# Kernel tuning notes

Measured on AMD Instinct MI355X. Metric: run time of the kernel, lower is better.

## Reference

```python
import jax, jax.numpy as jnp
import numpy as np

B, S, H, N = 4, 512, 768, 128
MAX_SPAN_WIDTH = 10
WIDTH_DIM = 30


def setup_inputs() -> dict:
    key = jax.random.key(0)
    ks = jax.random.split(key, 20)
    p = lambda k, shape: jax.random.normal(k, shape, jnp.float32) * 0.02
    starts = jax.random.randint(ks[1], (B, N), 0, S, dtype=jnp.int32)
    widths = jax.random.randint(ks[2], (B, N), 0, MAX_SPAN_WIDTH + 1, dtype=jnp.int32)
    ends = jnp.clip(starts + widths, 0, S - 1)
    return {
        "sequence_output": jax.random.normal(ks[0], (B, S, H), jnp.float32),
        "span_starts": starts,
        "span_ends": ends,
        # SpanRepresentation params (weights stored as [in, out], i.e. torch W.T)
        "W_start": p(ks[3], (H, H)), "b_start": p(ks[4], (H,)),
        "W_end": p(ks[5], (H, H)), "b_end": p(ks[6], (H,)),
        "width_emb": p(ks[7], (MAX_SPAN_WIDTH + 1, WIDTH_DIM)),
        "W_out": p(ks[8], (2 * H + WIDTH_DIM, H)), "b_out": p(ks[9], (H,)),
        # MentionScorer head
        "W_ment": p(ks[10], (H, 1)), "b_ment": p(ks[11], (1,)),
        # PairwiseScorer 2-layer MLP over concat([r_i, r_j, r_i - r_j])
        "W1": p(ks[12], (3 * H, H)), "b1": p(ks[13], (H,)),
        "W2": p(ks[14], (H, 1)), "b2": p(ks[15], (1,)),
    }


def reference(sequence_output, span_starts, span_ends,
              W_start, b_start, W_end, b_end, width_emb, W_out, b_out,
              W_ment, b_ment, W1, b1, W2, b2):
    bidx = jnp.arange(sequence_output.shape[0])[:, None]            # [B,1]
    # --- SpanRepresentation ---
    start_embed = sequence_output[bidx, span_starts] @ W_start + b_start  # [B,N,H]
    end_embed = sequence_output[bidx, span_ends] @ W_end + b_end          # [B,N,H]
    widths = jnp.clip(span_ends - span_starts, 0, MAX_SPAN_WIDTH)
    w_embed = width_emb[widths]                                           # [B,N,WD]
    span_repr = jnp.concatenate([start_embed, end_embed, w_embed], -1) @ W_out + b_out  # [B,N,H]
    # --- MentionScorer ---
    mention_scores = (span_repr @ W_ment + b_ment)[..., 0]               # [B,N]
    # --- PairwiseScorer: ffn(cat([r_i, r_j, r_i - r_j])) for j < i ---
    # cat([ri, rj, ri-rj]) @ W1 == ri@(Wa+Wc) + rj@(Wb-Wc), with W1 = [Wa;Wb;Wc]
    Wa, Wb, Wc = W1[:H], W1[H:2 * H], W1[2 * H:]
    Ai = span_repr @ (Wa + Wc)                                           # [B,N,H]
    Bj = span_repr @ (Wb - Wc)                                           # [B,N,H]
    hidden = jax.nn.relu(Ai[:, :, None, :] + Bj[:, None, :, :] + b1)     # [B,N,N,H]
    pw = (hidden @ W2)[..., 0] + b2[0]                                   # [B,N,N]
    lower = jnp.tril(jnp.ones((pw.shape[-1], pw.shape[-1]), bool), -1)
    pairwise_scores = jnp.where(lower, pw, jnp.zeros((), pw.dtype))
    return mention_scores, pairwise_scores
```

## Files before the change

kernel.cpp:

```cpp
#include <hip/hip_runtime.h>
#include <hip/hip_bf16.h>

#define H 768
#define K2P 1600
#define SEQLEN 512
#define NSPAN 128

typedef __attribute__((ext_vector_type(8))) short s16x8;
typedef __attribute__((ext_vector_type(4))) float f32x4;

#define MFMA_BF16 __builtin_amdgcn_mfma_f32_16x16x32_bf16

__device__ __forceinline__ short f2bf(float f) {
    __hip_bfloat16 h = __float2bfloat16(f);
    return *reinterpret_cast<short*>(&h);
}
__device__ __forceinline__ float bf2f(short s) {
    unsigned int u = ((unsigned int)(unsigned short)s) << 16;
    return __builtin_bit_cast(float, u);
}

#define SLOAD(P, K0)                                                           \
    P##0 = *(const s16x8*)(gA0 + (K0));                                        \
    P##1 = *(const s16x8*)(gA1 + (K0));                                        \
    P##2 = *(const s16x8*)(gB0 + (K0));                                        \
    P##3 = *(const s16x8*)(gB1 + (K0));

#define SWRITE(P, BUF)                                                         \
    *(s16x8*)((BUF) + dA0) = P##0;                                             \
    *(s16x8*)((BUF) + dA1) = P##1;                                             \
    *(s16x8*)((BUF) + dB0) = P##2;                                             \
    *(s16x8*)((BUF) + dB1) = P##3;

__device__ __forceinline__ void mstep32(const char* buf, int w, int r, int hi,
                                        f32x4& a0, f32x4& a1)
{
    #pragma unroll
    for (int kc = 0; kc < 2; ++kc) {
        const int ko = kc*64 + hi*16;
        const int ra0 = r, ra1 = 16 + r, rb = w*16 + r;
        s16x8 av0 = *(const s16x8*)(buf + ra0*128 + (ko ^ ((ra0 & 7) << 4)));
        s16x8 av1 = *(const s16x8*)(buf + ra1*128 + (ko ^ ((ra1 & 7) << 4)));
        s16x8 bv  = *(const s16x8*)(buf + 4096 + rb*128 + (ko ^ ((rb & 7) << 4)));
        a0 = MFMA_BF16(av0, bv, a0, 0, 0, 0);
        a1 = MFMA_BF16(av1, bv, a1, 0, 0, 0);
    }
}

__device__ __forceinline__ void gemm3232(
    short* ldsb,
    const short* __restrict__ A, int ldA, int am0,
    const short* __restrict__ Wt, int ldW, int n0,
    int nsteps, int tid,
    f32x4& a0, f32x4& a1)
{
    const int w = tid >> 6, l = tid & 63;
    const int r = l & 15, hi = l >> 4;

    const int rr = tid >> 3, sl = tid & 7;
    const short* gA0 = A + (size_t)(am0 + rr) * ldA + ((sl ^ (rr & 7)) << 3);
    const short* gA1 = A + (size_t)(am0 + rr + 16) * ldA + ((sl ^ (rr & 7)) << 3);
    const short* gB0 = Wt + (size_t)(n0 + rr) * ldW + ((sl ^ (rr & 7)) << 3);
    const short* gB1 = Wt + (size_t)(n0 + rr + 16) * ldW + ((sl ^ (rr & 7)) << 3);
    const int dA0 = rr*128 + sl*16,        dA1 = (rr+16)*128 + sl*16;
    const int dB0 = 4096 + rr*128 + sl*16, dB1 = 4096 + (rr+16)*128 + sl*16;
    char* b0 = (char*)ldsb;
    char* b1 = (char*)ldsb + 8192;

    s16x8 Pa0, Pa1, Pa2, Pa3;
    s16x8 Pb0, Pb1, Pb2, Pb3;

    SLOAD(Pa, 0)
    SWRITE(Pa, b0)
    SLOAD(Pa, 64)
    __syncthreads();
    for (int s = 0; s < nsteps; s += 2) {
        if (s + 2 < nsteps) { SLOAD(Pb, 64*(s+2)) }
        mstep32(b0, w, r, hi, a0, a1);
        if (s + 1 < nsteps) { SWRITE(Pa, b1) }
        __syncthreads();
        if (s + 1 < nsteps) {
            if (s + 3 < nsteps) { SLOAD(Pa, 64*(s+3)) }
            mstep32(b1, w, r, hi, a0, a1);
            if (s + 2 < nsteps) { SWRITE(Pb, b0) }
            __syncthreads();
        }
    }
}

__global__ __launch_bounds__(256) void k_prep(
    const float* __restrict__ seq,
    const int* __restrict__ starts, const int* __restrict__ ends,
    const float* __restrict__ Ws, const float* __restrict__ We,
    const float* __restrict__ W1, const float* __restrict__ Wout,
    const float* __restrict__ wemb,
    short* __restrict__ WtSE, short* __restrict__ WtAB,
    short* __restrict__ WtOut, short* __restrict__ Xg, short* __restrict__ Xcat)
{
    const int b = blockIdx.x;
    const int tid = threadIdx.x;

    if (b < 2304) {
        const int sec = b / 576;
        const int t = b % 576;
        const int kt = t / 24, nt = t % 24;
        __shared__ float tile[32][33];
        const int kk = tid >> 3;
        const int c4 = (tid & 7) << 2;
        const int srow = kt * 32 + kk, scol = nt * 32 + c4;
        float4 v;
        if (sec == 0)      v = *(const float4*)(Ws + (size_t)srow * H + scol);
        else if (sec == 1) v = *(const float4*)(We + (size_t)srow * H + scol);
        else {
            const float* base = W1 + (size_t)(sec == 2 ? 0 : H) * H;
            float4 u = *(const float4*)(base + (size_t)srow * H + scol);
            float4 c = *(const float4*)(W1 + (size_t)2*H*H + (size_t)srow * H + scol);
            const float sg = (sec == 2) ? 1.f : -1.f;
            v = make_float4(fmaf(sg,c.x,u.x), fmaf(sg,c.y,u.y),
                            fmaf(sg,c.z,u.z), fmaf(sg,c.w,u.w));
        }
        tile[kk][c4+0]=v.x; tile[kk][c4+1]=v.y; tile[kk][c4+2]=v.z; tile[kk][c4+3]=v.w;
        __syncthreads();
        short* dst = (sec < 2 ? WtSE : WtAB) + (size_t)(sec & 1) * H * H;
        const int nn = tid >> 3;
        short4 o;
        o.x = f2bf(tile[c4+0][nn]); o.y = f2bf(tile[c4+1][nn]);
        o.z = f2bf(tile[c4+2][nn]); o.w = f2bf(tile[c4+3][nn]);
        *(short4*)(dst + (size_t)(nt*32 + nn) * H + kt*32 + c4) = o;
    } else if (b < 3504) {
        const int t = b - 2304;
        const int nt = t / 50, kt = t % 50;
        __shared__ float tile[32][33];
        const int kk = tid >> 3;
        const int c4 = (tid & 7) << 2;
        const int srow = kt * 32 + kk, scol = nt * 32 + c4;
        float4 v = make_float4(0.f, 0.f, 0.f, 0.f);
        if (srow < 1566) v = *(const float4*)(Wout + (size_t)srow * H + scol);
        tile[kk][c4+0]=v.x; tile[kk][c4+1]=v.y; tile[kk][c4+2]=v.z; tile[kk][c4+3]=v.w;
        __syncthreads();
        const int nn = tid >> 3;
        short4 o;
        o.x = f2bf(tile[c4+0][nn]); o.y = f2bf(tile[c4+1][nn]);
        o.z = f2bf(tile[c4+2][nn]); o.w = f2bf(tile[c4+3][nn]);
        *(short4*)(WtOut + (size_t)(nt*32 + nn) * K2P + kt*32 + c4) = o;
    } else if (b < 3760) {
        const int gr = (b - 3504) * 4 + (tid >> 6);
        const int c = tid & 63;
        const int spanrow = gr & 511;
        const int idx = (gr < 512) ? starts[spanrow] : ends[spanrow];
        const size_t base = ((size_t)(spanrow >> 7) * SEQLEN + idx) * H;
        #pragma unroll
        for (int i = 0; i < 12; ++i) {
            const int col = c + i*64;
            Xg[(size_t)gr * H + col] = f2bf(seq[base + col]);
        }
    } else {
        const int t = (b - 3760) * 256 + tid;
        const int row = t >> 6, c = t & 63;
        int wd = ends[row] - starts[row];
        wd = wd < 0 ? 0 : (wd > 10 ? 10 : wd);
        Xcat[(size_t)row * K2P + 1536 + c] = (c < 30) ? f2bf(wemb[wd*30 + c]) : (short)0;
    }
}

__global__ __launch_bounds__(128) void k_g1(
    const short* __restrict__ Xg, const short* __restrict__ WtSE,
    const float* __restrict__ bs, const float* __restrict__ be,
    short* __restrict__ Xcat)
{
    __shared__ __align__(16) short lds[2][4096];
    const int tid = threadIdx.x;
    const int bm = blockIdx.x, n0 = blockIdx.y * 32;
    const int am0 = (n0 >= 768 ? 512 : 0) + bm * 32;

    f32x4 a0 = {}, a1 = {};
    gemm3232(&lds[0][0], Xg, H, am0, WtSE, H, n0, 12, tid, a0, a1);

    const int w = tid >> 6, l = tid & 63;
    const int r = l & 15, hi = l >> 4;
    const int gc = n0 + w*16 + r;
    const float bv = (gc < 768) ? bs[gc] : be[gc - 768];
    const int r0 = bm*32 + hi*4, r1 = r0 + 16;
    #pragma unroll
    for (int rg = 0; rg < 4; ++rg) {
        Xcat[(size_t)(r0 + rg) * K2P + gc] = f2bf(a0[rg] + bv);
        Xcat[(size_t)(r1 + rg) * K2P + gc] = f2bf(a1[rg] + bv);
    }
}

__global__ __launch_bounds__(128) void k_g2(
    const short* __restrict__ Xcat, const short* __restrict__ WtOut,
    const float* __restrict__ bout, short* __restrict__ SR)
{
    __shared__ __align__(16) short lds[2][4096];
    const int tid = threadIdx.x;
    const int bm = blockIdx.x, n0 = blockIdx.y * 32;

    f32x4 a0 = {}, a1 = {};
    gemm3232(&lds[0][0], Xcat, K2P, bm*32, WtOut, K2P, n0, 25, tid, a0, a1);

    const int w = tid >> 6, l = tid & 63;
    const int r = l & 15, hi = l >> 4;
    const int gc = n0 + w*16 + r;
    const float bv = bout[gc];
    const int r0 = bm*32 + hi*4, r1 = r0 + 16;
    #pragma unroll
    for (int rg = 0; rg < 4; ++rg) {
        SR[(size_t)(r0 + rg) * H + gc] = f2bf(a0[rg] + bv);
        SR[(size_t)(r1 + rg) * H + gc] = f2bf(a1[rg] + bv);
    }
}

__global__ __launch_bounds__(128) void k_g3(
    const short* __restrict__ SR, const short* __restrict__ WtAB,
    const float* __restrict__ b1, const float* __restrict__ Wm,
    const float* __restrict__ bment,
    float* __restrict__ AB, float* __restrict__ mention)
{
    const int tid = threadIdx.x;
    const int bm = blockIdx.x;

    if (blockIdx.y == 48) {
        const int w = tid >> 6, l = tid & 63;
        const int rows0 = bm*32 + w*16;
        const float bm_add = bment[0];
        for (int rr = 0; rr < 16; ++rr) {
            const int row = rows0 + rr;
            float p = 0.f;
            #pragma unroll
            for (int kk = 0; kk < 12; ++kk) {
                const int k = kk*64 + l;
                p = fmaf(bf2f(SR[(size_t)row * H + k]), Wm[k], p);
            }
            #pragma unroll
            for (int off = 32; off; off >>= 1) p += __shfl_down(p, off);
            if (l == 0) mention[row] = p + bm_add;
        }
        return;
    }

    __shared__ __align__(16) short lds[2][4096];
    const int n0 = blockIdx.y * 32;

    f32x4 a0 = {}, a1 = {};
    gemm3232(&lds[0][0], SR, H, bm*32, WtAB, H, n0, 12, tid, a0, a1);

    const int w = tid >> 6, l = tid & 63;
    const int r = l & 15, hi = l >> 4;
    const int gc = n0 + w*16 + r;
    const float bv = (gc < 768) ? b1[gc] : 0.f;
    const int r0 = bm*32 + hi*4, r1 = r0 + 16;
    #pragma unroll
    for (int rg = 0; rg < 4; ++rg) {
        AB[(size_t)(r0 + rg) * 1536 + gc] = a0[rg] + bv;
        AB[(size_t)(r1 + rg) * 1536 + gc] = a1[rg] + bv;
    }
}

__global__ __launch_bounds__(256) void k_pair(
    const float* __restrict__ AB, const float* __restrict__ W2,
    const float* __restrict__ b2, float* __restrict__ pair)
{
    const int tid = threadIdx.x;
    const int bx = blockIdx.x & 7, by = blockIdx.x >> 3;
    const int bz = blockIdx.y;

    const int tx = tid & 15, ty = tid >> 4;
    const int i = by * 16 + ty, j = bx * 16 + tx;
    float* outp = pair + ((size_t)bz * NSPAN + i) * NSPAN + j;

    if (bx > by) { *outp = 0.f; return; }

    __shared__ __align__(16) float Ais[16][68];
    __shared__ __align__(16) float Bjs[16][68];
    __shared__ __align__(16) float w2s[768];
    for (int q = tid; q < 768; q += 256) w2s[q] = W2[q];

    const int sr = tid >> 4, sc = (tid & 15) << 2;
    const float* aSrc = AB + ((size_t)bz*NSPAN + by*16 + sr)*1536 + sc;
    const float* bSrc = AB + ((size_t)bz*NSPAN + bx*16 + sr)*1536 + 768 + sc;
    float acc = 0.f;

    float4 ra = *(const float4*)(aSrc);
    float4 rb = *(const float4*)(bSrc);

    for (int ch = 0; ch < 12; ++ch) {
        __syncthreads();
        *(float4*)&Ais[sr][sc] = ra;
        *(float4*)&Bjs[sr][sc] = rb;
        __syncthreads();
        if (ch < 11) {
            ra = *(const float4*)(aSrc + (ch+1)*64);
            rb = *(const float4*)(bSrc + (ch+1)*64);
        }
        #pragma unroll
        for (int hq = 0; hq < 16; ++hq) {
            float4 a = *(const float4*)&Ais[ty][hq << 2];
            float4 b = *(const float4*)&Bjs[tx][hq << 2];
            float4 wv = *(const float4*)&w2s[ch*64 + (hq << 2)];
            acc = fmaf(fmaxf(a.x + b.x, 0.f), wv.x, acc);
            acc = fmaf(fmaxf(a.y + b.y, 0.f), wv.y, acc);
            acc = fmaf(fmaxf(a.z + b.z, 0.f), wv.z, acc);
            acc = fmaf(fmaxf(a.w + b.w, 0.f), wv.w, acc);
        }
    }
    *outp = (j < i) ? (acc + b2[0]) : 0.f;
}

extern "C" void kernel_launch(void* const* d_in, const int* in_sizes, int n_in,
                              void* d_out, int out_size, void* d_ws, size_t ws_size,
                              hipStream_t stream)
{
    const float* seq    = (const float*)d_in[0];
    const int*   starts = (const int*)  d_in[1];
    const int*   ends   = (const int*)  d_in[2];
    const float* Ws     = (const float*)d_in[3];
    const float* bs     = (const float*)d_in[4];
    const float* We     = (const float*)d_in[5];
    const float* be     = (const float*)d_in[6];
    const float* wemb   = (const float*)d_in[7];
    const float* Wout   = (const float*)d_in[8];
    const float* bout   = (const float*)d_in[9];
    const float* Wm     = (const float*)d_in[10];
    const float* bment  = (const float*)d_in[11];
    const float* W1     = (const float*)d_in[12];
    const float* b1     = (const float*)d_in[13];
    const float* W2     = (const float*)d_in[14];
    const float* b2     = (const float*)d_in[15];

    float* ws = (float*)d_ws;
    float* AB    = ws;
    short* Xg    = (short*)(ws + 786432);
    short* Xcat  = (short*)(ws + 1179648);
    short* SR    = (short*)(ws + 1589248);
    short* WtSE  = (short*)(ws + 1785856);
    short* WtAB  = (short*)(ws + 2375680);
    short* WtOut = (short*)(ws + 2965504);

    float* out_mention = (float*)d_out;
    float* out_pair    = (float*)d_out + 512;

    hipLaunchKernelGGL(k_prep, dim3(3888), dim3(256), 0, stream,
                       seq, starts, ends, Ws, We, W1, Wout, wemb,
                       WtSE, WtAB, WtOut, Xg, Xcat);
    hipLaunchKernelGGL(k_g1, dim3(16, 48), dim3(128), 0, stream,
                       Xg, WtSE, bs, be, Xcat);
    hipLaunchKernelGGL(k_g2, dim3(16, 24), dim3(128), 0, stream,
                       Xcat, WtOut, bout, SR);
    hipLaunchKernelGGL(k_g3, dim3(16, 49), dim3(128), 0, stream,
                       SR, WtAB, b1, Wm, bment, AB, out_mention);
    hipLaunchKernelGGL(k_pair, dim3(64, 4), dim3(256), 0, stream,
                       AB, W2, b2, out_pair);
}
```

Measured before the change: 46.90 us.

## Fuse span gather and start/end GEMM into prep kernel, dropping one launch

The start/end projection GEMM now reads fp32 sequence rows directly through the span indices and reads the fp32 Ws/We weights column-wise, converting to bf16 on the fly. This removes the separate gather into Xg, the transposed bf16 copies of Ws/We, and the k_g1 launch. The remaining prep work (W1 combination, Wout transpose, width embedding) runs in the same launch, which now uses 128-thread blocks. The cost is strided 8-element column loads of the weights inside the GEMM pipeline and uncoalesced fp32 traffic, in exchange for one fewer kernel boundary and less intermediate memory.

```diff
diff --git a/kernel.cpp b/kernel.cpp
--- a/kernel.cpp
+++ b/kernel.cpp
@@ -19,18 +19,18 @@
     unsigned int u = ((unsigned int)(unsigned short)s) << 16;
     return __builtin_bit_cast(float, u);
 }
-
-#define SLOAD(P, K0)                                                           \
-    P##0 = *(const s16x8*)(gA0 + (K0));                                        \
-    P##1 = *(const s16x8*)(gA1 + (K0));                                        \
-    P##2 = *(const s16x8*)(gB0 + (K0));                                        \
-    P##3 = *(const s16x8*)(gB1 + (K0));
-
-#define SWRITE(P, BUF)                                                         \
-    *(s16x8*)((BUF) + dA0) = P##0;                                             \
-    *(s16x8*)((BUF) + dA1) = P##1;                                             \
-    *(s16x8*)((BUF) + dB0) = P##2;                                             \
-    *(s16x8*)((BUF) + dB1) = P##3;
+__device__ __forceinline__ s16x8 cvt8(float4 v0, float4 v1) {
+    s16x8 r;
+    r[0] = f2bf(v0.x); r[1] = f2bf(v0.y); r[2] = f2bf(v0.z); r[3] = f2bf(v0.w);
+    r[4] = f2bf(v1.x); r[5] = f2bf(v1.y); r[6] = f2bf(v1.z); r[7] = f2bf(v1.w);
+    return r;
+}
+__device__ __forceinline__ s16x8 ldcol(const float* __restrict__ p) {
+    s16x8 t;
+    t[0] = f2bf(p[0*H]); t[1] = f2bf(p[1*H]); t[2] = f2bf(p[2*H]); t[3] = f2bf(p[3*H]);
+    t[4] = f2bf(p[4*H]); t[5] = f2bf(p[5*H]); t[6] = f2bf(p[6*H]); t[7] = f2bf(p[7*H]);
+    return t;
+}
 
 __device__ __forceinline__ void mstep32(const char* buf, int w, int r, int hi,
                                         f32x4& a0, f32x4& a1)
@@ -47,6 +47,18 @@
     }
 }
 
+#define SWRITE(P, BUF)                                                         \
+    *(s16x8*)((BUF) + dA0) = P##0;                                             \
+    *(s16x8*)((BUF) + dA1) = P##1;                                             \
+    *(s16x8*)((BUF) + dB0) = P##2;                                             \
+    *(s16x8*)((BUF) + dB1) = P##3;
+
+#define SLOAD(P, K0)                                                           \
+    P##0 = *(const s16x8*)(gA0 + (K0));                                        \
+    P##1 = *(const s16x8*)(gA1 + (K0));                                        \
+    P##2 = *(const s16x8*)(gB0 + (K0));                                        \
+    P##3 = *(const s16x8*)(gB1 + (K0));
+
 __device__ __forceinline__ void gemm3232(
     short* ldsb,
     const short* __restrict__ A, int ldA, int am0,
@@ -88,107 +100,154 @@
     }
 }
 
-__global__ __launch_bounds__(256) void k_prep(
+#define G1LOAD(P, K0)                                                          \
+    P##0 = cvt8(*(const float4*)(sA0 + (K0)), *(const float4*)(sA0 + (K0) + 4)); \
+    P##1 = cvt8(*(const float4*)(sA1 + (K0)), *(const float4*)(sA1 + (K0) + 4)); \
+    P##2 = ldcol(sB0 + (size_t)(K0) * H);                                      \
+    P##3 = ldcol(sB1 + (size_t)(K0) * H);
+
+__device__ __forceinline__ void g1pipe(
+    short* ldsb, const float* __restrict__ seq, const int* __restrict__ idx,
+    int bm, const float* __restrict__ W, int n0w, int tid,
+    f32x4& a0, f32x4& a1)
+{
+    const int w = tid >> 6, l = tid & 63;
+    const int r = l & 15, hi = l >> 4;
+
+    const int rr = tid >> 3, sl = tid & 7;
+    const int gm0 = bm*32 + rr, gm1 = gm0 + 16;
+    const float* sA0 = seq + ((size_t)((gm0 >> 7) * SEQLEN + idx[gm0])) * H
+                           + ((sl ^ (rr & 7)) << 3);
+    const float* sA1 = seq + ((size_t)((gm1 >> 7) * SEQLEN + idx[gm1])) * H
+                           + ((sl ^ (rr & 7)) << 3);
+    const int nl = tid & 31, ks0 = tid >> 5;
+    const float* sB0 = W + (size_t)(ks0 * 8) * H + n0w + nl;
+    const float* sB1 = W + (size_t)((ks0 + 4) * 8) * H + n0w + nl;
+    const int dA0 = rr*128 + sl*16, dA1 = (rr+16)*128 + sl*16;
+    const int dB0 = 4096 + nl*128 + ((ks0*16)     ^ ((nl & 7) << 4));
+    const int dB1 = 4096 + nl*128 + (((ks0+4)*16) ^ ((nl & 7) << 4));
+    char* b0 = (char*)ldsb;
+    char* b1 = (char*)ldsb + 8192;
+
+    s16x8 Pa0, Pa1, Pa2, Pa3;
+    s16x8 Pb0, Pb1, Pb2, Pb3;
+
+    G1LOAD(Pa, 0)
+    SWRITE(Pa, b0)
+    G1LOAD(Pa, 64)
+    __syncthreads();
+    for (int s = 0; s < 12; s += 2) {
+        if (s + 2 < 12) { G1LOAD(Pb, 64*(s+2)) }
+        mstep32(b0, w, r, hi, a0, a1);
+        SWRITE(Pa, b1)
+        __syncthreads();
+        {
+            if (s + 3 < 12) { G1LOAD(Pa, 64*(s+3)) }
+            mstep32(b1, w, r, hi, a0, a1);
+            if (s + 2 < 12) { SWRITE(Pb, b0) }
+            __syncthreads();
+        }
+    }
+}
+
+__global__ __launch_bounds__(128) void k1(
     const float* __restrict__ seq,
     const int* __restrict__ starts, const int* __restrict__ ends,
     const float* __restrict__ Ws, const float* __restrict__ We,
+    const float* __restrict__ bs, const float* __restrict__ be,
     const float* __restrict__ W1, const float* __restrict__ Wout,
     const float* __restrict__ wemb,
-    short* __restrict__ WtSE, short* __restrict__ WtAB,
-    short* __restrict__ WtOut, short* __restrict__ Xg, short* __restrict__ Xcat)
-{
-    const int b = blockIdx.x;
+    short* __restrict__ Xcat, short* __restrict__ WtAB,
+    short* __restrict__ WtOut)
+{
+    __shared__ __align__(16) short lds[2][4096];
+    const int bid = blockIdx.x;
     const int tid = threadIdx.x;
 
-    if (b < 2304) {
-        const int sec = b / 576;
-        const int t = b % 576;
+    if (bid < 768) {
+        const int bm = bid & 15, bn = bid >> 4;
+        const int n0 = bn * 32;
+        const int* idx = (n0 < 768) ? starts : ends;
+        const float* W = (n0 < 768) ? Ws : We;
+        const int n0w  = (n0 < 768) ? n0 : n0 - 768;
+
+        f32x4 a0 = {}, a1 = {};
+        g1pipe(&lds[0][0], seq, idx, bm, W, n0w, tid, a0, a1);
+
+        const int w = tid >> 6, l = tid & 63;
+        const int r = l & 15, hi = l >> 4;
+        const int gc = n0 + w*16 + r;
+        const float bv = (gc < 768) ? bs[gc] : be[gc - 768];
+        const int r0 = bm*32 + hi*4, r1 = r0 + 16;
+        #pragma unroll
+        for (int rg = 0; rg < 4; ++rg) {
+            Xcat[(size_t)(r0 + rg) * K2P + gc] = f2bf(a0[rg] + bv);
+            Xcat[(size_t)(r1 + rg) * K2P + gc] = f2bf(a1[rg] + bv);
+        }
+    } else if (bid < 1920) {
+        float (*tile)[33] = (float(*)[33])&lds[0][0];
+        const int sec = (bid - 768) / 576;
+        const int t = (bid - 768) % 576;
         const int kt = t / 24, nt = t % 24;
-        __shared__ float tile[32][33];
-        const int kk = tid >> 3;
         const int c4 = (tid & 7) << 2;
-        const int srow = kt * 32 + kk, scol = nt * 32 + c4;
-        float4 v;
-        if (sec == 0)      v = *(const float4*)(Ws + (size_t)srow * H + scol);
-        else if (sec == 1) v = *(const float4*)(We + (size_t)srow * H + scol);
-        else {
-            const float* base = W1 + (size_t)(sec == 2 ? 0 : H) * H;
+        const float* base = W1 + (size_t)(sec ? H : 0) * H;
+        const float sg = sec ? -1.f : 1.f;
+        #pragma unroll
+        for (int p = 0; p < 2; ++p) {
+            const int kk = p*16 + (tid >> 3);
+            const int srow = kt*32 + kk, scol = nt*32 + c4;
             float4 u = *(const float4*)(base + (size_t)srow * H + scol);
             float4 c = *(const float4*)(W1 + (size_t)2*H*H + (size_t)srow * H + scol);
-            const float sg = (sec == 2) ? 1.f : -1.f;
-            v = make_float4(fmaf(sg,c.x,u.x), fmaf(sg,c.y,u.y),
-                            fmaf(sg,c.z,u.z), fmaf(sg,c.w,u.w));
-        }
-        tile[kk][c4+0]=v.x; tile[kk][c4+1]=v.y; tile[kk][c4+2]=v.z; tile[kk][c4+3]=v.w;
-        __syncthreads();
-        short* dst = (sec < 2 ? WtSE : WtAB) + (size_t)(sec & 1) * H * H;
-        const int nn = tid >> 3;
-        short4 o;
-        o.x = f2bf(tile[c4+0][nn]); o.y = f2bf(tile[c4+1][nn]);
-        o.z = f2bf(tile[c4+2][nn]); o.w = f2bf(tile[c4+3][nn]);
-        *(short4*)(dst + (size_t)(nt*32 + nn) * H + kt*32 + c4) = o;
-    } else if (b < 3504) {
-        const int t = b - 2304;
+            tile[kk][c4+0] = fmaf(sg, c.x, u.x);
+            tile[kk][c4+1] = fmaf(sg, c.y, u.y);
+            tile[kk][c4+2] = fmaf(sg, c.z, u.z);
+            tile[kk][c4+3] = fmaf(sg, c.w, u.w);
+        }
+        __syncthreads();
+        short* dst = WtAB + (size_t)sec * H * H;
+        #pragma unroll
+        for (int p = 0; p < 2; ++p) {
+            const int nn = p*16 + (tid >> 3);
+            short4 o;
+            o.x = f2bf(tile[c4+0][nn]); o.y = f2bf(tile[c4+1][nn]);
+            o.z = f2bf(tile[c4+2][nn]); o.w = f2bf(tile[c4+3][nn]);
+            *(short4*)(dst + (size_t)(nt*32 + nn) * H + kt*32 + c4) = o;
+        }
+    } else if (bid < 3120) {
+        float (*tile)[33] = (float(*)[33])&lds[0][0];
+        const int t = bid - 1920;
         const int nt = t / 50, kt = t % 50;
-        __shared__ float tile[32][33];
-        const int kk = tid >> 3;
         const int c4 = (tid & 7) << 2;
-        const int srow = kt * 32 + kk, scol = nt * 32 + c4;
-        float4 v = make_float4(0.f, 0.f, 0.f, 0.f);
-        if (srow < 1566) v = *(const float4*)(Wout + (size_t)srow * H + scol);
-        tile[kk][c4+0]=v.x; tile[kk][c4+1]=v.y; tile[kk][c4+2]=v.z; tile[kk][c4+3]=v.w;
-        __syncthreads();
-        const int nn = tid >> 3;
-        short4 o;
-        o.x = f2bf(tile[c4+0][nn]); o.y = f2bf(tile[c4+1][nn]);
-        o.z = f2bf(tile[c4+2][nn]); o.w = f2bf(tile[c4+3][nn]);
-        *(short4*)(WtOut + (size_t)(nt*32 + nn) * K2P + kt*32 + c4) = o;
-    } else if (b < 3760) {
-        const int gr = (b - 3504) * 4 + (tid >> 6);
-        const int c = tid & 63;
-        const int spanrow = gr & 511;
-        const int idx = (gr < 512) ? starts[spanrow] : ends[spanrow];
-        const size_t base = ((size_t)(spanrow >> 7) * SEQLEN + idx) * H;
-        #pragma unroll
-        for (int i = 0; i < 12; ++i) {
-            const int col = c + i*64;
-            Xg[(size_t)gr * H + col] = f2bf(seq[base + col]);
+        #pragma unroll
+        for (int p = 0; p < 2; ++p) {
+            const int kk = p*16 + (tid >> 3);
+            const int srow = kt*32 + kk, scol = nt*32 + c4;
+            float4 v = make_float4(0.f, 0.f, 0.f, 0.f);
+            if (srow < 1566) v = *(const float4*)(Wout + (size_t)srow * H + scol);
+            tile[kk][c4+0] = v.x; tile[kk][c4+1] = v.y;
+            tile[kk][c4+2] = v.z; tile[kk][c4+3] = v.w;
+        }
+        __syncthreads();
+        #pragma unroll
+        for (int p = 0; p < 2; ++p) {
+            const int nn = p*16 + (tid >> 3);
+            short4 o;
+            o.x = f2bf(tile[c4+0][nn]); o.y = f2bf(tile[c4+1][nn]);
+            o.z = f2bf(tile[c4+2][nn]); o.w = f2bf(tile[c4+3][nn]);
+            *(short4*)(WtOut + (size_t)(nt*32 + nn) * K2P + kt*32 + c4) = o;
         }
     } else {
-        const int t = (b - 3760) * 256 + tid;
-        const int row = t >> 6, c = t & 63;
-        int wd = ends[row] - starts[row];
-        wd = wd < 0 ? 0 : (wd > 10 ? 10 : wd);
-        Xcat[(size_t)row * K2P + 1536 + c] = (c < 30) ? f2bf(wemb[wd*30 + c]) : (short)0;
-    }
-}
-
-__global__ __launch_bounds__(128) void k_g1(
-    const short* __restrict__ Xg, const short* __restrict__ WtSE,
-    const float* __restrict__ bs, const float* __restrict__ be,
-    short* __restrict__ Xcat)
-{
-    __shared__ __align__(16) short lds[2][4096];
-    const int tid = threadIdx.x;
-    const int bm = blockIdx.x, n0 = blockIdx.y * 32;
-    const int am0 = (n0 >= 768 ? 512 : 0) + bm * 32;
-
-    f32x4 a0 = {}, a1 = {};
-    gemm3232(&lds[0][0], Xg, H, am0, WtSE, H, n0, 12, tid, a0, a1);
-
-    const int w = tid >> 6, l = tid & 63;
-    const int r = l & 15, hi = l >> 4;
-    const int gc = n0 + w*16 + r;
-    const float bv = (gc < 768) ? bs[gc] : be[gc - 768];
-    const int r0 = bm*32 + hi*4, r1 = r0 + 16;
-    #pragma unroll
-    for (int rg = 0; rg < 4; ++rg) {
-        Xcat[(size_t)(r0 + rg) * K2P + gc] = f2bf(a0[rg] + bv);
-        Xcat[(size_t)(r1 + rg) * K2P + gc] = f2bf(a1[rg] + bv);
-    }
-}
-
-__global__ __launch_bounds__(128) void k_g2(
+        const int q = bid - 3120;
+        for (int t = tid; t < 32*64; t += 128) {
+            const int row = q*32 + (t >> 6), c = t & 63;
+            int wd = ends[row] - starts[row];
+            wd = wd < 0 ? 0 : (wd > 10 ? 10 : wd);
+            Xcat[(size_t)row * K2P + 1536 + c] = (c < 30) ? f2bf(wemb[wd*30 + c]) : (short)0;
+        }
+    }
+}
+
+__global__ __launch_bounds__(128) void k2(
     const short* __restrict__ Xcat, const short* __restrict__ WtOut,
     const float* __restrict__ bout, short* __restrict__ SR)
 {
@@ -211,7 +270,7 @@
     }
 }
 
-__global__ __launch_bounds__(128) void k_g3(
+__global__ __launch_bounds__(128) void k3(
     const short* __restrict__ SR, const short* __restrict__ WtAB,
     const float* __restrict__ b1, const float* __restrict__ Wm,
     const float* __restrict__ bment,
@@ -257,7 +316,7 @@
     }
 }
 
-__global__ __launch_bounds__(256) void k_pair(
+__global__ __launch_bounds__(256) void k4(
     const float* __restrict__ AB, const float* __restrict__ W2,
     const float* __restrict__ b2, float* __restrict__ pair)
 {
@@ -330,25 +389,21 @@
 
     float* ws = (float*)d_ws;
     float* AB    = ws;
-    short* Xg    = (short*)(ws + 786432);
-    short* Xcat  = (short*)(ws + 1179648);
-    short* SR    = (short*)(ws + 1589248);
-    short* WtSE  = (short*)(ws + 1785856);
-    short* WtAB  = (short*)(ws + 2375680);
-    short* WtOut = (short*)(ws + 2965504);
+    short* Xcat  = (short*)(ws + 786432);
+    short* SR    = Xcat + 819200;
+    short* WtAB  = SR + 393216;
+    short* WtOut = WtAB + 1179648;
 
     float* out_mention = (float*)d_out;
     float* out_pair    = (float*)d_out + 512;
 
-    hipLaunchKernelGGL(k_prep, dim3(3888), dim3(256), 0, stream,
-                       seq, starts, ends, Ws, We, W1, Wout, wemb,
-                       WtSE, WtAB, WtOut, Xg, Xcat);
-    hipLaunchKernelGGL(k_g1, dim3(16, 48), dim3(128), 0, stream,
-                       Xg, WtSE, bs, be, Xcat);
-    hipLaunchKernelGGL(k_g2, dim3(16, 24), dim3(128), 0, stream,
+    hipLaunchKernelGGL(k1, dim3(3136), dim3(128), 0, stream,
+                       seq, starts, ends, Ws, We, bs, be, W1, Wout, wemb,
+                       Xcat, WtAB, WtOut);
+    hipLaunchKernelGGL(k2, dim3(16, 24), dim3(128), 0, stream,
                        Xcat, WtOut, bout, SR);
-    hipLaunchKernelGGL(k_g3, dim3(16, 49), dim3(128), 0, stream,
+    hipLaunchKernelGGL(k3, dim3(16, 49), dim3(128), 0, stream,
                        SR, WtAB, b1, Wm, bment, AB, out_mention);
-    hipLaunchKernelGGL(k_pair, dim3(64, 4), dim3(256), 0, stream,
+    hipLaunchKernelGGL(k4, dim3(64, 4), dim3(256), 0, stream,
                        AB, W2, b2, out_pair);
 }
```

Result: slower. 49.22 us (+5.0%).

## Split GEMM K-loop across two thread halves with LDS reduction

Applied to the files above, without the earlier changes.

The three GEMM kernels now launch 256 threads per block. Each 128-thread half processes half of the K dimension with its own double-buffered LDS region, and the two partial accumulators are summed through LDS at the end. K2P is padded to 1664 so the Wout GEMM splits into two even halves, and the prep kernel's block ranges and workspace offsets are adjusted to match. The aim is to halve the serial K-loop per block and raise wave occupancy on these small GEMMs, at the cost of an extra reduction barrier and more padding work.

```diff
diff --git a/kernel.cpp b/kernel.cpp
--- a/kernel.cpp
+++ b/kernel.cpp
@@ -2,7 +2,7 @@
 #include <hip/hip_bf16.h>
 
 #define H 768
-#define K2P 1600
+#define K2P 1664
 #define SEQLEN 512
 #define NSPAN 128
 
@@ -19,18 +19,6 @@
     unsigned int u = ((unsigned int)(unsigned short)s) << 16;
     return __builtin_bit_cast(float, u);
 }
-
-#define SLOAD(P, K0)                                                           \
-    P##0 = *(const s16x8*)(gA0 + (K0));                                        \
-    P##1 = *(const s16x8*)(gA1 + (K0));                                        \
-    P##2 = *(const s16x8*)(gB0 + (K0));                                        \
-    P##3 = *(const s16x8*)(gB1 + (K0));
-
-#define SWRITE(P, BUF)                                                         \
-    *(s16x8*)((BUF) + dA0) = P##0;                                             \
-    *(s16x8*)((BUF) + dA1) = P##1;                                             \
-    *(s16x8*)((BUF) + dB0) = P##2;                                             \
-    *(s16x8*)((BUF) + dB1) = P##3;
 
 __device__ __forceinline__ void mstep32(const char* buf, int w, int r, int hi,
                                         f32x4& a0, f32x4& a1)
@@ -47,25 +35,39 @@
     }
 }
 
-__device__ __forceinline__ void gemm3232(
+#define SLOAD(P, K0)                                                           \
+    P##0 = *(const s16x8*)(gA0 + (K0));                                        \
+    P##1 = *(const s16x8*)(gA1 + (K0));                                        \
+    P##2 = *(const s16x8*)(gB0 + (K0));                                        \
+    P##3 = *(const s16x8*)(gB1 + (K0));
+
+#define SWRITE(P, BUF)                                                         \
+    *(s16x8*)((BUF) + dA0) = P##0;                                             \
+    *(s16x8*)((BUF) + dA1) = P##1;                                             \
+    *(s16x8*)((BUF) + dB0) = P##2;                                             \
+    *(s16x8*)((BUF) + dB1) = P##3;
+
+__device__ __forceinline__ void gemm_sk(
     short* ldsb,
     const short* __restrict__ A, int ldA, int am0,
     const short* __restrict__ Wt, int ldW, int n0,
-    int nsteps, int tid,
+    int halfsteps, int tid,
     f32x4& a0, f32x4& a1)
 {
-    const int w = tid >> 6, l = tid & 63;
+    const int pr = tid >> 7, pt = tid & 127;
+    const int w = pt >> 6, l = pt & 63;
     const int r = l & 15, hi = l >> 4;
-
-    const int rr = tid >> 3, sl = tid & 7;
-    const short* gA0 = A + (size_t)(am0 + rr) * ldA + ((sl ^ (rr & 7)) << 3);
-    const short* gA1 = A + (size_t)(am0 + rr + 16) * ldA + ((sl ^ (rr & 7)) << 3);
-    const short* gB0 = Wt + (size_t)(n0 + rr) * ldW + ((sl ^ (rr & 7)) << 3);
-    const short* gB1 = Wt + (size_t)(n0 + rr + 16) * ldW + ((sl ^ (rr & 7)) << 3);
+    const int kof = pr * halfsteps * 64;
+
+    const int rr = pt >> 3, sl = pt & 7;
+    const short* gA0 = A + (size_t)(am0 + rr) * ldA + kof + ((sl ^ (rr & 7)) << 3);
+    const short* gA1 = A + (size_t)(am0 + rr + 16) * ldA + kof + ((sl ^ (rr & 7)) << 3);
+    const short* gB0 = Wt + (size_t)(n0 + rr) * ldW + kof + ((sl ^ (rr & 7)) << 3);
+    const short* gB1 = Wt + (size_t)(n0 + rr + 16) * ldW + kof + ((sl ^ (rr & 7)) << 3);
     const int dA0 = rr*128 + sl*16,        dA1 = (rr+16)*128 + sl*16;
     const int dB0 = 4096 + rr*128 + sl*16, dB1 = 4096 + (rr+16)*128 + sl*16;
-    char* b0 = (char*)ldsb;
-    char* b1 = (char*)ldsb + 8192;
+    char* b0 = (char*)ldsb + pr*16384;
+    char* b1 = b0 + 8192;
 
     s16x8 Pa0, Pa1, Pa2, Pa3;
     s16x8 Pb0, Pb1, Pb2, Pb3;
@@ -74,17 +76,27 @@
     SWRITE(Pa, b0)
     SLOAD(Pa, 64)
     __syncthreads();
-    for (int s = 0; s < nsteps; s += 2) {
-        if (s + 2 < nsteps) { SLOAD(Pb, 64*(s+2)) }
+    for (int s = 0; s < halfsteps; s += 2) {
+        if (s + 2 < halfsteps) { SLOAD(Pb, 64*(s+2)) }
         mstep32(b0, w, r, hi, a0, a1);
-        if (s + 1 < nsteps) { SWRITE(Pa, b1) }
-        __syncthreads();
-        if (s + 1 < nsteps) {
-            if (s + 3 < nsteps) { SLOAD(Pa, 64*(s+3)) }
+        if (s + 1 < halfsteps) { SWRITE(Pa, b1) }
+        __syncthreads();
+        if (s + 1 < halfsteps) {
+            if (s + 3 < halfsteps) { SLOAD(Pa, 64*(s+3)) }
             mstep32(b1, w, r, hi, a0, a1);
-            if (s + 2 < nsteps) { SWRITE(Pb, b0) }
+            if (s + 2 < halfsteps) { SWRITE(Pb, b0) }
             __syncthreads();
         }
+    }
+    float* red = (float*)ldsb;
+    if (pr) {
+        *(f32x4*)(red + pt*8)     = a0;
+        *(f32x4*)(red + pt*8 + 4) = a1;
+    }
+    __syncthreads();
+    if (!pr) {
+        a0 += *(const f32x4*)(red + pt*8);
+        a1 += *(const f32x4*)(red + pt*8 + 4);
     }
 }
 
@@ -127,9 +139,9 @@
         o.x = f2bf(tile[c4+0][nn]); o.y = f2bf(tile[c4+1][nn]);
         o.z = f2bf(tile[c4+2][nn]); o.w = f2bf(tile[c4+3][nn]);
         *(short4*)(dst + (size_t)(nt*32 + nn) * H + kt*32 + c4) = o;
-    } else if (b < 3504) {
+    } else if (b < 3552) {
         const int t = b - 2304;
-        const int nt = t / 50, kt = t % 50;
+        const int nt = t / 52, kt = t % 52;
         __shared__ float tile[32][33];
         const int kk = tid >> 3;
         const int c4 = (tid & 7) << 2;
@@ -143,8 +155,8 @@
         o.x = f2bf(tile[c4+0][nn]); o.y = f2bf(tile[c4+1][nn]);
         o.z = f2bf(tile[c4+2][nn]); o.w = f2bf(tile[c4+3][nn]);
         *(short4*)(WtOut + (size_t)(nt*32 + nn) * K2P + kt*32 + c4) = o;
-    } else if (b < 3760) {
-        const int gr = (b - 3504) * 4 + (tid >> 6);
+    } else if (b < 3808) {
+        const int gr = (b - 3552) * 4 + (tid >> 6);
         const int c = tid & 63;
         const int spanrow = gr & 511;
         const int idx = (gr < 512) ? starts[spanrow] : ends[spanrow];
@@ -155,63 +167,69 @@
             Xg[(size_t)gr * H + col] = f2bf(seq[base + col]);
         }
     } else {
-        const int t = (b - 3760) * 256 + tid;
-        const int row = t >> 6, c = t & 63;
-        int wd = ends[row] - starts[row];
-        wd = wd < 0 ? 0 : (wd > 10 ? 10 : wd);
-        Xcat[(size_t)row * K2P + 1536 + c] = (c < 30) ? f2bf(wemb[wd*30 + c]) : (short)0;
-    }
-}
-
-__global__ __launch_bounds__(128) void k_g1(
+        const int q = b - 3808;
+        for (int t = tid; t < 32*128; t += 256) {
+            const int row = q*32 + (t >> 7), c = t & 127;
+            int wd = ends[row] - starts[row];
+            wd = wd < 0 ? 0 : (wd > 10 ? 10 : wd);
+            Xcat[(size_t)row * K2P + 1536 + c] = (c < 30) ? f2bf(wemb[wd*30 + c]) : (short)0;
+        }
+    }
+}
+
+__global__ __launch_bounds__(256) void k_g1(
     const short* __restrict__ Xg, const short* __restrict__ WtSE,
     const float* __restrict__ bs, const float* __restrict__ be,
     short* __restrict__ Xcat)
 {
-    __shared__ __align__(16) short lds[2][4096];
+    __shared__ __align__(16) short lds[4][4096];
     const int tid = threadIdx.x;
     const int bm = blockIdx.x, n0 = blockIdx.y * 32;
     const int am0 = (n0 >= 768 ? 512 : 0) + bm * 32;
 
     f32x4 a0 = {}, a1 = {};
-    gemm3232(&lds[0][0], Xg, H, am0, WtSE, H, n0, 12, tid, a0, a1);
-
-    const int w = tid >> 6, l = tid & 63;
-    const int r = l & 15, hi = l >> 4;
-    const int gc = n0 + w*16 + r;
-    const float bv = (gc < 768) ? bs[gc] : be[gc - 768];
-    const int r0 = bm*32 + hi*4, r1 = r0 + 16;
-    #pragma unroll
-    for (int rg = 0; rg < 4; ++rg) {
-        Xcat[(size_t)(r0 + rg) * K2P + gc] = f2bf(a0[rg] + bv);
-        Xcat[(size_t)(r1 + rg) * K2P + gc] = f2bf(a1[rg] + bv);
-    }
-}
-
-__global__ __launch_bounds__(128) void k_g2(
+    gemm_sk(&lds[0][0], Xg, H, am0, WtSE, H, n0, 6, tid, a0, a1);
+
+    if (tid < 128) {
+        const int w = tid >> 6, l = tid & 63;
+        const int r = l & 15, hi = l >> 4;
+        const int gc = n0 + w*16 + r;
+        const float bv = (gc < 768) ? bs[gc] : be[gc - 768];
+        const int r0 = bm*32 + hi*4, r1 = r0 + 16;
+        #pragma unroll
+        for (int rg = 0; rg < 4; ++rg) {
+            Xcat[(size_t)(r0 + rg) * K2P + gc] = f2bf(a0[rg] + bv);
+            Xcat[(size_t)(r1 + rg) * K2P + gc] = f2bf(a1[rg] + bv);
+        }
+    }
+}
+
+__global__ __launch_bounds__(256) void k_g2(
     const short* __restrict__ Xcat, const short* __restrict__ WtOut,
     const float* __restrict__ bout, short* __restrict__ SR)
 {
-    __shared__ __align__(16) short lds[2][4096];
+    __shared__ __align__(16) short lds[4][4096];
     const int tid = threadIdx.x;
     const int bm = blockIdx.x, n0 = blockIdx.y * 32;
 
     f32x4 a0 = {}, a1 = {};
-    gemm3232(&lds[0][0], Xcat, K2P, bm*32, WtOut, K2P, n0, 25, tid, a0, a1);
-
-    const int w = tid >> 6, l = tid & 63;
-    const int r = l & 15, hi = l >> 4;
-    const int gc = n0 + w*16 + r;
-    const float bv = bout[gc];
-    const int r0 = bm*32 + hi*4, r1 = r0 + 16;
-    #pragma unroll
-    for (int rg = 0; rg < 4; ++rg) {
-        SR[(size_t)(r0 + rg) * H + gc] = f2bf(a0[rg] + bv);
-        SR[(size_t)(r1 + rg) * H + gc] = f2bf(a1[rg] + bv);
-    }
-}
-
-__global__ __launch_bounds__(128) void k_g3(
+    gemm_sk(&lds[0][0], Xcat, K2P, bm*32, WtOut, K2P, n0, 13, tid, a0, a1);
+
+    if (tid < 128) {
+        const int w = tid >> 6, l = tid & 63;
+        const int r = l & 15, hi = l >> 4;
+        const int gc = n0 + w*16 + r;
+        const float bv = bout[gc];
+        const int r0 = bm*32 + hi*4, r1 = r0 + 16;
+        #pragma unroll
+        for (int rg = 0; rg < 4; ++rg) {
+            SR[(size_t)(r0 + rg) * H + gc] = f2bf(a0[rg] + bv);
+            SR[(size_t)(r1 + rg) * H + gc] = f2bf(a1[rg] + bv);
+        }
+    }
+}
+
+__global__ __launch_bounds__(256) void k_g3(
     const short* __restrict__ SR, const short* __restrict__ WtAB,
     const float* __restrict__ b1, const float* __restrict__ Wm,
     const float* __restrict__ bment,
@@ -221,10 +239,10 @@
     const int bm = blockIdx.x;
 
     if (blockIdx.y == 48) {
-        const int w = tid >> 6, l = tid & 63;
-        const int rows0 = bm*32 + w*16;
+        const int w4 = tid >> 6, l = tid & 63;
+        const int rows0 = bm*32 + w4*8;
         const float bm_add = bment[0];
-        for (int rr = 0; rr < 16; ++rr) {
+        for (int rr = 0; rr < 8; ++rr) {
             const int row = rows0 + rr;
             float p = 0.f;
             #pragma unroll
@@ -239,21 +257,23 @@
         return;
     }
 
-    __shared__ __align__(16) short lds[2][4096];
+    __shared__ __align__(16) short lds[4][4096];
     const int n0 = blockIdx.y * 32;
 
     f32x4 a0 = {}, a1 = {};
-    gemm3232(&lds[0][0], SR, H, bm*32, WtAB, H, n0, 12, tid, a0, a1);
-
-    const int w = tid >> 6, l = tid & 63;
-    const int r = l & 15, hi = l >> 4;
-    const int gc = n0 + w*16 + r;
-    const float bv = (gc < 768) ? b1[gc] : 0.f;
-    const int r0 = bm*32 + hi*4, r1 = r0 + 16;
-    #pragma unroll
-    for (int rg = 0; rg < 4; ++rg) {
-        AB[(size_t)(r0 + rg) * 1536 + gc] = a0[rg] + bv;
-        AB[(size_t)(r1 + rg) * 1536 + gc] = a1[rg] + bv;
+    gemm_sk(&lds[0][0], SR, H, bm*32, WtAB, H, n0, 6, tid, a0, a1);
+
+    if (tid < 128) {
+        const int w = tid >> 6, l = tid & 63;
+        const int r = l & 15, hi = l >> 4;
+        const int gc = n0 + w*16 + r;
+        const float bv = (gc < 768) ? b1[gc] : 0.f;
+        const int r0 = bm*32 + hi*4, r1 = r0 + 16;
+        #pragma unroll
+        for (int rg = 0; rg < 4; ++rg) {
+            AB[(size_t)(r0 + rg) * 1536 + gc] = a0[rg] + bv;
+            AB[(size_t)(r1 + rg) * 1536 + gc] = a1[rg] + bv;
+        }
     }
 }
 
@@ -331,23 +351,23 @@
     float* ws = (float*)d_ws;
     float* AB    = ws;
     short* Xg    = (short*)(ws + 786432);
-    short* Xcat  = (short*)(ws + 1179648);
-    short* SR    = (short*)(ws + 1589248);
-    short* WtSE  = (short*)(ws + 1785856);
-    short* WtAB  = (short*)(ws + 2375680);
-    short* WtOut = (short*)(ws + 2965504);
+    short* Xcat  = Xg + 786432;
+    short* SR    = Xcat + 851968;
+    short* WtSE  = SR + 393216;
+    short* WtAB  = WtSE + 1179648;
+    short* WtOut = WtAB + 1179648;
 
     float* out_mention = (float*)d_out;
     float* out_pair    = (float*)d_out + 512;
 
-    hipLaunchKernelGGL(k_prep, dim3(3888), dim3(256), 0, stream,
+    hipLaunchKernelGGL(k_prep, dim3(3824), dim3(256), 0, stream,
                        seq, starts, ends, Ws, We, W1, Wout, wemb,
                        WtSE, WtAB, WtOut, Xg, Xcat);
-    hipLaunchKernelGGL(k_g1, dim3(16, 48), dim3(128), 0, stream,
+    hipLaunchKernelGGL(k_g1, dim3(16, 48), dim3(256), 0, stream,
                        Xg, WtSE, bs, be, Xcat);
-    hipLaunchKernelGGL(k_g2, dim3(16, 24), dim3(128), 0, stream,
+    hipLaunchKernelGGL(k_g2, dim3(16, 24), dim3(256), 0, stream,
                        Xcat, WtOut, bout, SR);
-    hipLaunchKernelGGL(k_g3, dim3(16, 49), dim3(128), 0, stream,
+    hipLaunchKernelGGL(k_g3, dim3(16, 49), dim3(256), 0, stream,
                        SR, WtAB, b1, Wm, bment, AB, out_mention);
     hipLaunchKernelGGL(k_pair, dim3(64, 4), dim3(256), 0, stream,
                        AB, W2, b2, out_pair);
```

Result: slower. 48.36 us (+3.1%).

## Precompute width-embedding projection table and drop the padded K tail from span GEMM

Applied to the files above, without the earlier changes.

The width-embedding contribution (width_emb @ W_out rows 1536..1565 plus the bias) is precomputed once as an 11x768 fp32 table in the prep kernel. The output GEMM then adds a table row selected by each span's width in its epilogue. This shrinks that GEMM's K from 1600 to 1536, removes the padded Xcat tail writes, and keeps that part in fp32. The cost is a single prep block that serially computes the table, which may lengthen the prep kernel's tail.

```diff
diff --git a/kernel.cpp b/kernel.cpp
--- a/kernel.cpp
+++ b/kernel.cpp
@@ -2,7 +2,7 @@
 #include <hip/hip_bf16.h>
 
 #define H 768
-#define K2P 1600
+#define LDX 1536
 #define SEQLEN 512
 #define NSPAN 128
 
@@ -19,18 +19,6 @@
     unsigned int u = ((unsigned int)(unsigned short)s) << 16;
     return __builtin_bit_cast(float, u);
 }
-
-#define SLOAD(P, K0)                                                           \
-    P##0 = *(const s16x8*)(gA0 + (K0));                                        \
-    P##1 = *(const s16x8*)(gA1 + (K0));                                        \
-    P##2 = *(const s16x8*)(gB0 + (K0));                                        \
-    P##3 = *(const s16x8*)(gB1 + (K0));
-
-#define SWRITE(P, BUF)                                                         \
-    *(s16x8*)((BUF) + dA0) = P##0;                                             \
-    *(s16x8*)((BUF) + dA1) = P##1;                                             \
-    *(s16x8*)((BUF) + dB0) = P##2;                                             \
-    *(s16x8*)((BUF) + dB1) = P##3;
 
 __device__ __forceinline__ void mstep32(const char* buf, int w, int r, int hi,
                                         f32x4& a0, f32x4& a1)
@@ -47,6 +35,18 @@
     }
 }
 
+#define SLOAD(P, K0)                                                           \
+    P##0 = *(const s16x8*)(gA0 + (K0));                                        \
+    P##1 = *(const s16x8*)(gA1 + (K0));                                        \
+    P##2 = *(const s16x8*)(gB0 + (K0));                                        \
+    P##3 = *(const s16x8*)(gB1 + (K0));
+
+#define SWRITE(P, BUF)                                                         \
+    *(s16x8*)((BUF) + dA0) = P##0;                                             \
+    *(s16x8*)((BUF) + dA1) = P##1;                                             \
+    *(s16x8*)((BUF) + dB0) = P##2;                                             \
+    *(s16x8*)((BUF) + dB1) = P##3;
+
 __device__ __forceinline__ void gemm3232(
     short* ldsb,
     const short* __restrict__ A, int ldA, int am0,
@@ -93,9 +93,10 @@
     const int* __restrict__ starts, const int* __restrict__ ends,
     const float* __restrict__ Ws, const float* __restrict__ We,
     const float* __restrict__ W1, const float* __restrict__ Wout,
-    const float* __restrict__ wemb,
+    const float* __restrict__ wemb, const float* __restrict__ bout,
     short* __restrict__ WtSE, short* __restrict__ WtAB,
-    short* __restrict__ WtOut, short* __restrict__ Xg, short* __restrict__ Xcat)
+    short* __restrict__ WtOut, short* __restrict__ Xg,
+    float* __restrict__ Tbl)
 {
     const int b = blockIdx.x;
     const int tid = threadIdx.x;
@@ -127,24 +128,23 @@
         o.x = f2bf(tile[c4+0][nn]); o.y = f2bf(tile[c4+1][nn]);
         o.z = f2bf(tile[c4+2][nn]); o.w = f2bf(tile[c4+3][nn]);
         *(short4*)(dst + (size_t)(nt*32 + nn) * H + kt*32 + c4) = o;
-    } else if (b < 3504) {
+    } else if (b < 3456) {
         const int t = b - 2304;
-        const int nt = t / 50, kt = t % 50;
+        const int nt = t / 48, kt = t % 48;
         __shared__ float tile[32][33];
         const int kk = tid >> 3;
         const int c4 = (tid & 7) << 2;
         const int srow = kt * 32 + kk, scol = nt * 32 + c4;
-        float4 v = make_float4(0.f, 0.f, 0.f, 0.f);
-        if (srow < 1566) v = *(const float4*)(Wout + (size_t)srow * H + scol);
+        float4 v = *(const float4*)(Wout + (size_t)srow * H + scol);
         tile[kk][c4+0]=v.x; tile[kk][c4+1]=v.y; tile[kk][c4+2]=v.z; tile[kk][c4+3]=v.w;
         __syncthreads();
         const int nn = tid >> 3;
         short4 o;
         o.x = f2bf(tile[c4+0][nn]); o.y = f2bf(tile[c4+1][nn]);
         o.z = f2bf(tile[c4+2][nn]); o.w = f2bf(tile[c4+3][nn]);
-        *(short4*)(WtOut + (size_t)(nt*32 + nn) * K2P + kt*32 + c4) = o;
-    } else if (b < 3760) {
-        const int gr = (b - 3504) * 4 + (tid >> 6);
+        *(short4*)(WtOut + (size_t)(nt*32 + nn) * LDX + kt*32 + c4) = o;
+    } else if (b < 3712) {
+        const int gr = (b - 3456) * 4 + (tid >> 6);
         const int c = tid & 63;
         const int spanrow = gr & 511;
         const int idx = (gr < 512) ? starts[spanrow] : ends[spanrow];
@@ -155,11 +155,23 @@
             Xg[(size_t)gr * H + col] = f2bf(seq[base + col]);
         }
     } else {
-        const int t = (b - 3760) * 256 + tid;
-        const int row = t >> 6, c = t & 63;
-        int wd = ends[row] - starts[row];
-        wd = wd < 0 ? 0 : (wd > 10 ? 10 : wd);
-        Xcat[(size_t)row * K2P + 1536 + c] = (c < 30) ? f2bf(wemb[wd*30 + c]) : (short)0;
+        __shared__ float we_s[11*30];
+        for (int t = tid; t < 11*30; t += 256) we_s[t] = wemb[t];
+        __syncthreads();
+        for (int n = tid; n < 768; n += 256) {
+            float wcol[30];
+            #pragma unroll
+            for (int k = 0; k < 30; ++k)
+                wcol[k] = Wout[(size_t)(1536 + k) * H + n];
+            const float bv = bout[n];
+            for (int wd = 0; wd < 11; ++wd) {
+                float s = bv;
+                #pragma unroll
+                for (int k = 0; k < 30; ++k)
+                    s = fmaf(we_s[wd*30 + k], wcol[k], s);
+                Tbl[wd*768 + n] = s;
+            }
+        }
     }
 }
 
@@ -183,31 +195,35 @@
     const int r0 = bm*32 + hi*4, r1 = r0 + 16;
     #pragma unroll
     for (int rg = 0; rg < 4; ++rg) {
-        Xcat[(size_t)(r0 + rg) * K2P + gc] = f2bf(a0[rg] + bv);
-        Xcat[(size_t)(r1 + rg) * K2P + gc] = f2bf(a1[rg] + bv);
+        Xcat[(size_t)(r0 + rg) * LDX + gc] = f2bf(a0[rg] + bv);
+        Xcat[(size_t)(r1 + rg) * LDX + gc] = f2bf(a1[rg] + bv);
     }
 }
 
 __global__ __launch_bounds__(128) void k_g2(
     const short* __restrict__ Xcat, const short* __restrict__ WtOut,
-    const float* __restrict__ bout, short* __restrict__ SR)
+    const int* __restrict__ starts, const int* __restrict__ ends,
+    const float* __restrict__ Tbl, short* __restrict__ SR)
 {
     __shared__ __align__(16) short lds[2][4096];
     const int tid = threadIdx.x;
     const int bm = blockIdx.x, n0 = blockIdx.y * 32;
 
     f32x4 a0 = {}, a1 = {};
-    gemm3232(&lds[0][0], Xcat, K2P, bm*32, WtOut, K2P, n0, 25, tid, a0, a1);
+    gemm3232(&lds[0][0], Xcat, LDX, bm*32, WtOut, LDX, n0, 24, tid, a0, a1);
 
     const int w = tid >> 6, l = tid & 63;
     const int r = l & 15, hi = l >> 4;
     const int gc = n0 + w*16 + r;
-    const float bv = bout[gc];
     const int r0 = bm*32 + hi*4, r1 = r0 + 16;
     #pragma unroll
     for (int rg = 0; rg < 4; ++rg) {
-        SR[(size_t)(r0 + rg) * H + gc] = f2bf(a0[rg] + bv);
-        SR[(size_t)(r1 + rg) * H + gc] = f2bf(a1[rg] + bv);
+        int wd0 = ends[r0+rg] - starts[r0+rg];
+        wd0 = wd0 < 0 ? 0 : (wd0 > 10 ? 10 : wd0);
+        int wd1 = ends[r1+rg] - starts[r1+rg];
+        wd1 = wd1 < 0 ? 0 : (wd1 > 10 ? 10 : wd1);
+        SR[(size_t)(r0 + rg) * H + gc] = f2bf(a0[rg] + Tbl[wd0*768 + gc]);
+        SR[(size_t)(r1 + rg) * H + gc] = f2bf(a1[rg] + Tbl[wd1*768 + gc]);
     }
 }
 
@@ -331,22 +347,23 @@
     float* ws = (float*)d_ws;
     float* AB    = ws;
     short* Xg    = (short*)(ws + 786432);
-    short* Xcat  = (short*)(ws + 1179648);
-    short* SR    = (short*)(ws + 1589248);
-    short* WtSE  = (short*)(ws + 1785856);
-    short* WtAB  = (short*)(ws + 2375680);
-    short* WtOut = (short*)(ws + 2965504);
+    short* Xcat  = Xg + 786432;
+    short* SR    = Xcat + 786432;
+    short* WtSE  = SR + 393216;
+    short* WtAB  = WtSE + 1179648;
+    short* WtOut = WtAB + 1179648;
+    float* Tbl   = (float*)(WtOut + 1179648);
 
     float* out_mention = (float*)d_out;
     float* out_pair    = (float*)d_out + 512;
 
-    hipLaunchKernelGGL(k_prep, dim3(3888), dim3(256), 0, stream,
-                       seq, starts, ends, Ws, We, W1, Wout, wemb,
-                       WtSE, WtAB, WtOut, Xg, Xcat);
+    hipLaunchKernelGGL(k_prep, dim3(3713), dim3(256), 0, stream,
+                       seq, starts, ends, Ws, We, W1, Wout, wemb, bout,
+                       WtSE, WtAB, WtOut, Xg, Tbl);
     hipLaunchKernelGGL(k_g1, dim3(16, 48), dim3(128), 0, stream,
                        Xg, WtSE, bs, be, Xcat);
     hipLaunchKernelGGL(k_g2, dim3(16, 24), dim3(128), 0, stream,
-                       Xcat, WtOut, bout, SR);
+                       Xcat, WtOut, starts, ends, Tbl, SR);
     hipLaunchKernelGGL(k_g3, dim3(16, 49), dim3(128), 0, stream,
                        SR, WtAB, b1, Wm, bment, AB, out_mention);
     hipLaunchKernelGGL(k_pair, dim3(64, 4), dim3(256), 0, stream,
```

New measurement: 62.07 us. 1.32x slower.
